# Kernel tuning notes

Hardware: AMD Instinct MI355X
Metric: run time of the kernel (lower is better)

Reference implementation:

```python
import jax, jax.numpy as jnp
import numpy as np

N = 100000      # nodes
E = 1600000     # edges (avg degree 16)
IN, HID, OUT = 128, 32, 64
H = 4           # attention heads in hidden layers

def _p(key, shape, scale=0.1):
    return jax.random.normal(key, shape, dtype=jnp.float32) * scale

def setup_inputs():
    key = jax.random.key(0)
    ks = jax.random.split(key, 16)
    return {
        "x": jax.random.normal(ks[0], (N, IN), dtype=jnp.float32),
        "edge_index": jax.random.randint(ks[1], (2, E), 0, N, dtype=jnp.int32),
        # layer 1: GATConv(IN -> HID, heads=4, concat=True) + BN
        "W1": _p(ks[2], (IN, H * HID)), "as1": _p(ks[3], (H, HID)), "ad1": _p(ks[4], (H, HID)),
        "b1": jnp.zeros((H * HID,), jnp.float32),
        "g1": jnp.ones((H * HID,), jnp.float32), "be1": jnp.zeros((H * HID,), jnp.float32),
        "rm1": _p(ks[5], (H * HID,)), "rv1": jnp.ones((H * HID,), jnp.float32),
        # layer 2: GATConv(H*HID -> HID, heads=4, concat=True) + BN
        "W2": _p(ks[6], (H * HID, H * HID)), "as2": _p(ks[7], (H, HID)), "ad2": _p(ks[8], (H, HID)),
        "b2": jnp.zeros((H * HID,), jnp.float32),
        "g2": jnp.ones((H * HID,), jnp.float32), "be2": jnp.zeros((H * HID,), jnp.float32),
        "rm2": _p(ks[9], (H * HID,)), "rv2": jnp.ones((H * HID,), jnp.float32),
        # layer 3: GATConv(H*HID -> OUT, heads=1, concat=False)
        "W3": _p(ks[10], (H * HID, OUT)), "as3": _p(ks[11], (1, OUT)), "ad3": _p(ks[12], (1, OUT)),
        "b3": jnp.zeros((OUT,), jnp.float32),
    }

def _gat(x, W, a_s, a_d, b, src, dst, heads, ch, concat):
    n = x.shape[0]
    h = (x @ W).reshape(n, heads, ch)                        # [N,H,C]
    e = (h * a_s).sum(-1)[src] + (h * a_d).sum(-1)[dst]      # per-edge logits [E,H]
    e = jax.nn.leaky_relu(e, 0.2)
    m = jax.ops.segment_max(e, dst, num_segments=n)          # segment softmax over dst
    ex = jnp.exp(e - m[dst])
    den = jax.ops.segment_sum(ex, dst, num_segments=n)
    alpha = ex / den[dst]                                    # self loops guarantee den > 0
    out = jax.ops.segment_sum(h[src] * alpha[:, :, None], dst, num_segments=n)
    out = out.reshape(n, heads * ch) if concat else out.mean(axis=1)
    return out + b

def _bn(x, g, b, rm, rv):                                    # BatchNorm1d, eval mode
    return (x - rm) * jax.lax.rsqrt(rv + 1e-5) * g + b

def _forward(x, edge_index, W1, as1, ad1, b1, g1, be1, rm1, rv1,
             W2, as2, ad2, b2, g2, be2, rm2, rv2, W3, as3, ad3, b3):
    n = x.shape[0]
    loop = jnp.arange(n, dtype=edge_index.dtype)             # add self loops (PyG default)
    src = jnp.concatenate([edge_index[0], loop])
    dst = jnp.concatenate([edge_index[1], loop])
    h = _gat(x, W1, as1, ad1, b1, src, dst, H, HID, True)
    h = jax.nn.elu(_bn(h, g1, be1, rm1, rv1))                # dropout = identity (eval)
    h = _gat(h, W2, as2, ad2, b2, src, dst, H, HID, True)
    h = jax.nn.elu(_bn(h, g2, be2, rm2, rv2))
    return _gat(h, W3, as3, ad3, b3, src, dst, 1, OUT, False)

def reference(x, edge_index, W1, as1, ad1, b1, g1, be1, rm1, rv1,
              W2, as2, ad2, b2, g2, be2, rm2, rv2, W3, as3, ad3, b3):
    return _forward(x, edge_index, W1, as1, ad1, b1, g1, be1, rm1, rv1,
                    W2, as2, ad2, b2, g2, be2, rm2, rv2, W3, as3, ad3, b3)
```

## Files before the change

### kernel.cpp

```cpp
#include <hip/hip_runtime.h>
#include <hip/hip_fp16.h>

#define CDIV(a,b) (((a)+(b)-1)/(b))

typedef _Float16 f16x8 __attribute__((ext_vector_type(8)));
typedef float f32x4 __attribute__((ext_vector_type(4)));

__global__ __launch_bounds__(256) void conv_kernel(const float* __restrict__ X,
                                                   __half* __restrict__ Y, int total4) {
  int t = blockIdx.x * blockDim.x + threadIdx.x;
  if (t >= total4) return;
  float4 v = reinterpret_cast<const float4*>(X)[t];
  __half2 a = __floats2half2_rn(v.x, v.y);
  __half2 b = __floats2half2_rn(v.z, v.w);
  reinterpret_cast<__half2*>(Y)[t * 2]     = a;
  reinterpret_cast<__half2*>(Y)[t * 2 + 1] = b;
}

__global__ __launch_bounds__(256) void wprep_kernel(const float* __restrict__ W,
                                                    _Float16* __restrict__ Wt, int NOUT) {
  int i = blockIdx.x * blockDim.x + threadIdx.x;
  if (i >= 128 * NOUT) return;
  int k = i / NOUT, c = i % NOUT;
  int s = k >> 5, g = (k >> 3) & 3, e = k & 7;
  Wt[(size_t)((s * 4 + g) * NOUT + c) * 8 + e] = (_Float16)W[i];
}

template<int NOUT>
__global__ __launch_bounds__(256) void gemm_mfma(const __half* __restrict__ Xh,
                                                 const _Float16* __restrict__ Wt,
                                                 __half* __restrict__ Y, int nrows) {
  constexpr int K = 128;
  constexpr int CT = NOUT / 16;
  const int wave = threadIdx.x >> 6, lane = threadIdx.x & 63;
  const int g = lane >> 4, r16 = lane & 15;
  const int rt = blockIdx.x * 4 + wave;
  if (rt * 16 >= nrows) return;

  const _Float16* xrow = reinterpret_cast<const _Float16*>(Xh)
                         + (size_t)(rt * 16 + r16) * K + g * 8;
  f16x8 a[4];
  #pragma unroll
  for (int s = 0; s < 4; ++s) a[s] = *reinterpret_cast<const f16x8*>(xrow + s * 32);

  f32x4 acc[CT];
  #pragma unroll
  for (int ct = 0; ct < CT; ++ct) acc[ct] = (f32x4){0.f, 0.f, 0.f, 0.f};

  #pragma unroll
  for (int ct = 0; ct < CT; ++ct) {
    #pragma unroll
    for (int s = 0; s < 4; ++s) {
      f16x8 b = *reinterpret_cast<const f16x8*>(&Wt[(size_t)((s * 4 + g) * NOUT + ct * 16 + r16) * 8]);
      acc[ct] = __builtin_amdgcn_mfma_f32_16x16x32_f16(a[s], b, acc[ct], 0, 0, 0);
    }
  }
  const int row0 = rt * 16 + g * 4;
  #pragma unroll
  for (int ct = 0; ct < CT; ++ct) {
    #pragma unroll
    for (int r = 0; r < 4; ++r) {
      Y[(size_t)(row0 + r) * NOUT + ct * 16 + r16] = __float2half_rn(acc[ct][r]);
    }
  }
}

template<int HEADS, int CH>
__global__ __launch_bounds__(256) void scores_kernel(const __half* __restrict__ Hf,
                                                     const float* __restrict__ as_,
                                                     const float* __restrict__ ad_,
                                                     float* __restrict__ ssrc,
                                                     float* __restrict__ sdst, int n) {
  int t = blockIdx.x * blockDim.x + threadIdx.x;
  if (t >= n * HEADS) return;
  int hd = t % HEADS;
  const __half2* hp2 = reinterpret_cast<const __half2*>(Hf + (size_t)t * CH);
  float a = 0.f, b = 0.f;
  #pragma unroll
  for (int c2 = 0; c2 < CH / 2; ++c2) {
    float2 v = __half22float2(hp2[c2]);
    a += v.x * as_[hd * CH + 2 * c2] + v.y * as_[hd * CH + 2 * c2 + 1];
    b += v.x * ad_[hd * CH + 2 * c2] + v.y * ad_[hd * CH + 2 * c2 + 1];
  }
  ssrc[t] = a; sdst[t] = b;
}

__global__ __launch_bounds__(256) void hist_kernel(const int* __restrict__ ei, int E,
                                                   int* __restrict__ deg) {
  int e = blockIdx.x * blockDim.x + threadIdx.x;
  if (e >= E) return;
  atomicAdd(&deg[ei[E + e]], 1);
}

__global__ __launch_bounds__(256) void scan_blocksums(const int* __restrict__ deg,
                                                      int* __restrict__ bsum, int N) {
  __shared__ int red[256];
  int base = blockIdx.x * 1024 + threadIdx.x * 4;
  int s = 0;
  #pragma unroll
  for (int i = 0; i < 4; ++i) { int idx = base + i; if (idx < N) s += deg[idx]; }
  red[threadIdx.x] = s;
  __syncthreads();
  for (int off = 128; off > 0; off >>= 1) {
    if (threadIdx.x < off) red[threadIdx.x] += red[threadIdx.x + off];
    __syncthreads();
  }
  if (threadIdx.x == 0) bsum[blockIdx.x] = red[0];
}

__global__ __launch_bounds__(1024) void scan_bsum(int* __restrict__ bsum, int nb) {
  __shared__ int sh[1024];
  int t = threadIdx.x;
  int v = (t < nb) ? bsum[t] : 0;
  sh[t] = v;
  __syncthreads();
  for (int off = 1; off < 1024; off <<= 1) {
    int tmp = (t >= off) ? sh[t - off] : 0;
    __syncthreads();
    sh[t] += tmp;
    __syncthreads();
  }
  if (t < nb) bsum[t] = sh[t] - v;
}

__global__ __launch_bounds__(256) void scan_final(const int* __restrict__ deg,
                                                  const int* __restrict__ bsum,
                                                  int* __restrict__ rowptr,
                                                  int* __restrict__ cursor, int N) {
  __shared__ int sh[256];
  const int t = threadIdx.x;
  const int base = blockIdx.x * 1024 + t * 4;
  int d[4] = {0, 0, 0, 0};
  #pragma unroll
  for (int i = 0; i < 4; ++i) if (base + i < N) d[i] = deg[base + i];
  int s = d[0] + d[1] + d[2] + d[3];
  sh[t] = s;
  __syncthreads();
  for (int off = 1; off < 256; off <<= 1) {
    int tmp = (t >= off) ? sh[t - off] : 0;
    __syncthreads();
    sh[t] += tmp;
    __syncthreads();
  }
  int run = bsum[blockIdx.x] + sh[t] - s;
  #pragma unroll
  for (int i = 0; i < 4; ++i) {
    if (base + i < N) { rowptr[base + i] = run; cursor[base + i] = run; run += d[i]; }
  }
  if (blockIdx.x == gridDim.x - 1 && t == 255) rowptr[N] = run;
}

__global__ __launch_bounds__(256) void scatter_pass(const int* __restrict__ ei, int E, int N,
                                                    int pw,
                                                    int* __restrict__ cursor,
                                                    int* __restrict__ col) {
  int e = blockIdx.x * blockDim.x + threadIdx.x;
  if (e >= E) return;
  int lo = blockIdx.y * pw;
  int hi = lo + pw;
  int d = ei[E + e];
  if (d < lo || d >= hi) return;
  int pos = atomicAdd(&cursor[d], 1);
  col[pos] = ei[e];
}

template<int HEADS, int CH, bool BN, bool OUTH>
__global__ __launch_bounds__(256) void gat_fused(
    const int* __restrict__ rowptr, const int* __restrict__ col,
    const __half* __restrict__ Hf,
    const float* __restrict__ ssrc, const float* __restrict__ sdst,
    const float* __restrict__ bias, const float* __restrict__ g,
    const float* __restrict__ be, const float* __restrict__ rm,
    const float* __restrict__ rv,
    void* __restrict__ outp, int N) {
  constexpr int NOUT = HEADS * CH;
  constexpr int VEC = NOUT / 64;
  constexpr int SLOTS = 64 / HEADS;
  __shared__ float ptile[4][SLOTS][HEADS];
  __shared__ int   stile[4][SLOTS];
  const int wv = threadIdx.x >> 6, lane = threadIdx.x & 63;
  const int n = blockIdx.x * 4 + wv;
  if (n >= N) return;
  const int eslot = lane / HEADS, head = lane & (HEADS - 1);
  const float sd = sdst[n * HEADS + head];
  float lgs = ssrc[n * HEADS + head] + sd;
  lgs = lgs > 0.f ? lgs : 0.2f * lgs;

  const int c0 = lane * VEC;
  const int hb = c0 / CH;

  float a0, a1 = 0.f;
  if (VEC == 2) {
    float2 hf = __half22float2(*reinterpret_cast<const __half2*>(&Hf[(size_t)n * NOUT + c0]));
    a0 = hf.x; a1 = hf.y;
  } else {
    a0 = __half2float(Hf[(size_t)n * NOUT + c0]);
  }

  float s = 0.f;
  const int beg = rowptr[n], end = rowptr[n + 1];
  for (int base = beg; base < end; base += SLOTS) {
    int e = base + eslot;
    float p = 0.f; int src = 0;
    if (e < end) {
      src = col[e];
      float lg = ssrc[src * HEADS + head] + sd;
      lg = lg > 0.f ? lg : 0.2f * lg;
      p = __expf(lg - lgs);
    }
    ptile[wv][eslot][head] = p;
    if (head == 0) stile[wv][eslot] = src;
    s += p;
    asm volatile("s_waitcnt lgkmcnt(0)" ::: "memory");

    int cnt = min(SLOTS, end - base);
    if (cnt == SLOTS) {
      #pragma unroll 16
      for (int j = 0; j < SLOTS; ++j) {
        int sj = stile[wv][j];
        float pj = ptile[wv][j][hb];
        if (VEC == 2) {
          float2 hf = __half22float2(*reinterpret_cast<const __half2*>(&Hf[(size_t)sj * NOUT + c0]));
          a0 += pj * hf.x; a1 += pj * hf.y;
        } else {
          a0 += pj * __half2float(Hf[(size_t)sj * NOUT + c0]);
        }
      }
    } else {
      for (int j = 0; j < cnt; ++j) {
        int sj = stile[wv][j];
        float pj = ptile[wv][j][hb];
        if (VEC == 2) {
          float2 hf = __half22float2(*reinterpret_cast<const __half2*>(&Hf[(size_t)sj * NOUT + c0]));
          a0 += pj * hf.x; a1 += pj * hf.y;
        } else {
          a0 += pj * __half2float(Hf[(size_t)sj * NOUT + c0]);
        }
      }
    }
  }

  #pragma unroll
  for (int off = HEADS; off < 64; off <<= 1) s += __shfl_xor(s, off);
  float inv = 1.f / (s + 1.f);
  float invb = __shfl(inv, hb);

  float o0 = a0 * invb + bias[c0];
  if (BN) {
    o0 = (o0 - rm[c0]) * rsqrtf(rv[c0] + 1e-5f) * g[c0] + be[c0];
    o0 = o0 > 0.f ? o0 : expm1f(o0);
  }
  if (VEC == 2) {
    float o1 = a1 * invb + bias[c0 + 1];
    if (BN) {
      o1 = (o1 - rm[c0 + 1]) * rsqrtf(rv[c0 + 1] + 1e-5f) * g[c0 + 1] + be[c0 + 1];
      o1 = o1 > 0.f ? o1 : expm1f(o1);
    }
    if (OUTH) {
      __half2 o = __floats2half2_rn(o0, o1);
      *reinterpret_cast<__half2*>(&((__half*)outp)[(size_t)n * NOUT + c0]) = o;
    } else {
      float2 o = make_float2(o0, o1);
      *reinterpret_cast<float2*>(&((float*)outp)[(size_t)n * NOUT + c0]) = o;
    }
  } else {
    if (OUTH) ((__half*)outp)[(size_t)n * NOUT + c0] = __float2half_rn(o0);
    else      ((float*)outp)[(size_t)n * NOUT + c0] = o0;
  }
}

extern "C" void kernel_launch(void* const* d_in, const int* in_sizes, int n_in,
                              void* d_out, int out_size, void* d_ws, size_t ws_size,
                              hipStream_t stream) {
  const float* x   = (const float*)d_in[0];
  const int*   ei  = (const int*)d_in[1];
  const float* W1  = (const float*)d_in[2];
  const float* as1 = (const float*)d_in[3];
  const float* ad1 = (const float*)d_in[4];
  const float* b1  = (const float*)d_in[5];
  const float* g1  = (const float*)d_in[6];
  const float* be1 = (const float*)d_in[7];
  const float* rm1 = (const float*)d_in[8];
  const float* rv1 = (const float*)d_in[9];
  const float* W2  = (const float*)d_in[10];
  const float* as2 = (const float*)d_in[11];
  const float* ad2 = (const float*)d_in[12];
  const float* b2  = (const float*)d_in[13];
  const float* g2  = (const float*)d_in[14];
  const float* be2 = (const float*)d_in[15];
  const float* rm2 = (const float*)d_in[16];
  const float* rv2 = (const float*)d_in[17];
  const float* W3  = (const float*)d_in[18];
  const float* as3 = (const float*)d_in[19];
  const float* ad3 = (const float*)d_in[20];
  const float* b3  = (const float*)d_in[21];

  const int N = in_sizes[0] / 128;
  const int E = in_sizes[1] / 2;
  float* out = (float*)d_out;

  char* p = (char*)d_ws;
  __half* Ah  = (__half*)p;  p += (size_t)N * 128 * 2;
  __half* Bh  = (__half*)p;  p += (size_t)N * 128 * 2;
  float* ssrc = (float*)p;   p += (size_t)N * 4 * 4;
  float* sdst = (float*)p;   p += (size_t)N * 4 * 4;
  int* deg    = (int*)p;     p += (size_t)N * 4;
  int* rowptr = (int*)p;     p += (size_t)(N + 1) * 4;
  int* cursor = (int*)p;     p += (size_t)N * 4;
  int* col    = (int*)p;     p += (size_t)E * 4;
  int* bsum   = (int*)p;     p += 4096;
  _Float16* Wt1 = (_Float16*)p; p += (size_t)128 * 128 * 2;
  _Float16* Wt2 = (_Float16*)p; p += (size_t)128 * 128 * 2;
  _Float16* Wt3 = (_Float16*)p;

  const int fusedB = CDIV(N, 4);
  const int nb = CDIV(N, 1024);
  const int gemmB = CDIV(N, 64);
  constexpr int NPASS = 8;
  const int pw = CDIV(N, NPASS);

  hipMemsetAsync(deg, 0, (size_t)N * sizeof(int), stream);
  hist_kernel<<<CDIV(E, 256), 256, 0, stream>>>(ei, E, deg);
  scan_blocksums<<<nb, 256, 0, stream>>>(deg, bsum, N);
  scan_bsum<<<1, 1024, 0, stream>>>(bsum, nb);
  scan_final<<<nb, 256, 0, stream>>>(deg, bsum, rowptr, cursor, N);
  scatter_pass<<<dim3(CDIV(E, 256), NPASS), 256, 0, stream>>>(ei, E, N, pw, cursor, col);

  wprep_kernel<<<CDIV(128 * 128, 256), 256, 0, stream>>>(W1, Wt1, 128);
  wprep_kernel<<<CDIV(128 * 128, 256), 256, 0, stream>>>(W2, Wt2, 128);
  wprep_kernel<<<CDIV(128 * 64, 256), 256, 0, stream>>>(W3, Wt3, 64);
  conv_kernel<<<CDIV(N * 128 / 4, 256), 256, 0, stream>>>(x, Bh, N * 128 / 4);

  gemm_mfma<128><<<gemmB, 256, 0, stream>>>(Bh, Wt1, Ah, N);
  scores_kernel<4, 32><<<CDIV(N * 4, 256), 256, 0, stream>>>(Ah, as1, ad1, ssrc, sdst, N);
  gat_fused<4, 32, true, true><<<fusedB, 256, 0, stream>>>(rowptr, col, Ah, ssrc, sdst,
                                                           b1, g1, be1, rm1, rv1, Bh, N);

  gemm_mfma<128><<<gemmB, 256, 0, stream>>>(Bh, Wt2, Ah, N);
  scores_kernel<4, 32><<<CDIV(N * 4, 256), 256, 0, stream>>>(Ah, as2, ad2, ssrc, sdst, N);
  gat_fused<4, 32, true, true><<<fusedB, 256, 0, stream>>>(rowptr, col, Ah, ssrc, sdst,
                                                           b2, g2, be2, rm2, rv2, Bh, N);

  gemm_mfma<64><<<gemmB, 256, 0, stream>>>(Bh, Wt3, Ah, N);
  scores_kernel<1, 64><<<CDIV(N, 256), 256, 0, stream>>>(Ah, as3, ad3, ssrc, sdst, N);
  gat_fused<1, 64, false, false><<<fusedB, 256, 0, stream>>>(rowptr, col, Ah, ssrc, sdst,
                                                             b3, b3, b3, b3, b3, out, N);
}
```

Baseline: 489.8 us.

## Fuse score computation into GEMM, fold fp32 conversion, and restructure aggregation with shuffles

The attention-score dot products move into the MFMA GEMM epilogue, computed from the accumulators with cross-lane shuffle reductions. This removes the separate scores kernels and the re-read of the projected features. The layer-1 GEMM now reads fp32 input directly, which drops the standalone conversion kernel, and the three weight-prep launches are merged into one. The aggregation kernel replaces LDS tiles with register shuffles and splits each wave into two halves that process alternate edges with wider per-lane loads, adding the self term at the end; this trades LDS traffic for more shuffles and a final cross-half reduction.

```diff
diff --git a/kernel.cpp b/kernel.cpp
--- a/kernel.cpp
+++ b/kernel.cpp
@@ -1,47 +1,63 @@
 #include <hip/hip_runtime.h>
 #include <hip/hip_fp16.h>
+#include <type_traits>
 
 #define CDIV(a,b) (((a)+(b)-1)/(b))
 
 typedef _Float16 f16x8 __attribute__((ext_vector_type(8)));
 typedef float f32x4 __attribute__((ext_vector_type(4)));
 
-__global__ __launch_bounds__(256) void conv_kernel(const float* __restrict__ X,
-                                                   __half* __restrict__ Y, int total4) {
-  int t = blockIdx.x * blockDim.x + threadIdx.x;
-  if (t >= total4) return;
-  float4 v = reinterpret_cast<const float4*>(X)[t];
-  __half2 a = __floats2half2_rn(v.x, v.y);
-  __half2 b = __floats2half2_rn(v.z, v.w);
-  reinterpret_cast<__half2*>(Y)[t * 2]     = a;
-  reinterpret_cast<__half2*>(Y)[t * 2 + 1] = b;
-}
-
-__global__ __launch_bounds__(256) void wprep_kernel(const float* __restrict__ W,
-                                                    _Float16* __restrict__ Wt, int NOUT) {
-  int i = blockIdx.x * blockDim.x + threadIdx.x;
-  if (i >= 128 * NOUT) return;
+__device__ __forceinline__ void wxform(const float* __restrict__ W,
+                                       _Float16* __restrict__ Wt, int i, int NOUT) {
   int k = i / NOUT, c = i % NOUT;
   int s = k >> 5, g = (k >> 3) & 3, e = k & 7;
   Wt[(size_t)((s * 4 + g) * NOUT + c) * 8 + e] = (_Float16)W[i];
 }
-
-template<int NOUT>
-__global__ __launch_bounds__(256) void gemm_mfma(const __half* __restrict__ Xh,
-                                                 const _Float16* __restrict__ Wt,
-                                                 __half* __restrict__ Y, int nrows) {
+__global__ __launch_bounds__(256) void wprep_all(const float* __restrict__ W1,
+                                                 const float* __restrict__ W2,
+                                                 const float* __restrict__ W3,
+                                                 _Float16* __restrict__ Wt1,
+                                                 _Float16* __restrict__ Wt2,
+                                                 _Float16* __restrict__ Wt3) {
+  int i = blockIdx.x * blockDim.x + threadIdx.x;
+  if (i < 128 * 128) { wxform(W1, Wt1, i, 128); wxform(W2, Wt2, i, 128); }
+  if (i < 128 * 64)  { wxform(W3, Wt3, i, 64); }
+}
+
+template<typename AT>
+__device__ __forceinline__ f16x8 load_afrag(const AT* __restrict__ xrow) {
+  if constexpr (std::is_same<AT, _Float16>::value) {
+    return *reinterpret_cast<const f16x8*>(xrow);
+  } else {
+    float4 v0 = *reinterpret_cast<const float4*>(xrow);
+    float4 v1 = *reinterpret_cast<const float4*>(xrow + 4);
+    f16x8 r = {(_Float16)v0.x, (_Float16)v0.y, (_Float16)v0.z, (_Float16)v0.w,
+               (_Float16)v1.x, (_Float16)v1.y, (_Float16)v1.z, (_Float16)v1.w};
+    return r;
+  }
+}
+
+template<int NOUT, int HEADS, typename AT>
+__global__ __launch_bounds__(256) void gemm_sc(const AT* __restrict__ X,
+                                               const _Float16* __restrict__ Wt,
+                                               const float* __restrict__ as_,
+                                               const float* __restrict__ ad_,
+                                               __half* __restrict__ Y,
+                                               float* __restrict__ ssrc,
+                                               float* __restrict__ sdst, int nrows) {
   constexpr int K = 128;
   constexpr int CT = NOUT / 16;
+  constexpr int CH = NOUT / HEADS;
+  constexpr int CPH = CH / 16;
   const int wave = threadIdx.x >> 6, lane = threadIdx.x & 63;
   const int g = lane >> 4, r16 = lane & 15;
   const int rt = blockIdx.x * 4 + wave;
   if (rt * 16 >= nrows) return;
 
-  const _Float16* xrow = reinterpret_cast<const _Float16*>(Xh)
-                         + (size_t)(rt * 16 + r16) * K + g * 8;
+  const AT* xrow = X + (size_t)(rt * 16 + r16) * K + g * 8;
   f16x8 a[4];
   #pragma unroll
-  for (int s = 0; s < 4; ++s) a[s] = *reinterpret_cast<const f16x8*>(xrow + s * 32);
+  for (int s = 0; s < 4; ++s) a[s] = load_afrag(xrow + s * 32);
 
   f32x4 acc[CT];
   #pragma unroll
@@ -63,26 +79,47 @@
       Y[(size_t)(row0 + r) * NOUT + ct * 16 + r16] = __float2half_rn(acc[ct][r]);
     }
   }
-}
-
-template<int HEADS, int CH>
-__global__ __launch_bounds__(256) void scores_kernel(const __half* __restrict__ Hf,
-                                                     const float* __restrict__ as_,
-                                                     const float* __restrict__ ad_,
-                                                     float* __restrict__ ssrc,
-                                                     float* __restrict__ sdst, int n) {
-  int t = blockIdx.x * blockDim.x + threadIdx.x;
-  if (t >= n * HEADS) return;
-  int hd = t % HEADS;
-  const __half2* hp2 = reinterpret_cast<const __half2*>(Hf + (size_t)t * CH);
-  float a = 0.f, b = 0.f;
-  #pragma unroll
-  for (int c2 = 0; c2 < CH / 2; ++c2) {
-    float2 v = __half22float2(hp2[c2]);
-    a += v.x * as_[hd * CH + 2 * c2] + v.y * as_[hd * CH + 2 * c2 + 1];
-    b += v.x * ad_[hd * CH + 2 * c2] + v.y * ad_[hd * CH + 2 * c2 + 1];
-  }
-  ssrc[t] = a; sdst[t] = b;
+
+  float pas[4][HEADS], pad_[4][HEADS];
+  #pragma unroll
+  for (int r = 0; r < 4; ++r)
+    #pragma unroll
+    for (int h = 0; h < HEADS; ++h) { pas[r][h] = 0.f; pad_[r][h] = 0.f; }
+  #pragma unroll
+  for (int h = 0; h < HEADS; ++h) {
+    #pragma unroll
+    for (int q = 0; q < CPH; ++q) {
+      float asv = as_[h * CH + q * 16 + r16];
+      float adv = ad_[h * CH + q * 16 + r16];
+      #pragma unroll
+      for (int r = 0; r < 4; ++r) {
+        float av = acc[h * CPH + q][r];
+        pas[r][h] += av * asv;
+        pad_[r][h] += av * adv;
+      }
+    }
+  }
+  #pragma unroll
+  for (int off = 1; off < 16; off <<= 1) {
+    #pragma unroll
+    for (int r = 0; r < 4; ++r)
+      #pragma unroll
+      for (int h = 0; h < HEADS; ++h) {
+        pas[r][h] += __shfl_xor(pas[r][h], off);
+        pad_[r][h] += __shfl_xor(pad_[r][h], off);
+      }
+  }
+  #pragma unroll
+  for (int h = 0; h < HEADS; ++h) {
+    if (r16 == h) {
+      #pragma unroll
+      for (int r = 0; r < 4; ++r) ssrc[(size_t)(row0 + r) * HEADS + h] = pas[r][h];
+    }
+    if (r16 == 8 + h) {
+      #pragma unroll
+      for (int r = 0; r < 4; ++r) sdst[(size_t)(row0 + r) * HEADS + h] = pad_[r][h];
+    }
+  }
 }
 
 __global__ __launch_bounds__(256) void hist_kernel(const int* __restrict__ ei, int E,
@@ -165,7 +202,7 @@
 }
 
 template<int HEADS, int CH, bool BN, bool OUTH>
-__global__ __launch_bounds__(256) void gat_fused(
+__global__ __launch_bounds__(256) void gat_fused2(
     const int* __restrict__ rowptr, const int* __restrict__ col,
     const __half* __restrict__ Hf,
     const float* __restrict__ ssrc, const float* __restrict__ sdst,
@@ -174,98 +211,100 @@
     const float* __restrict__ rv,
     void* __restrict__ outp, int N) {
   constexpr int NOUT = HEADS * CH;
-  constexpr int VEC = NOUT / 64;
   constexpr int SLOTS = 64 / HEADS;
-  __shared__ float ptile[4][SLOTS][HEADS];
-  __shared__ int   stile[4][SLOTS];
+  constexpr int CPL = NOUT / 32;
   const int wv = threadIdx.x >> 6, lane = threadIdx.x & 63;
   const int n = blockIdx.x * 4 + wv;
   if (n >= N) return;
   const int eslot = lane / HEADS, head = lane & (HEADS - 1);
+  const int half_ = lane >> 5, li = lane & 31;
+  const int c0 = li * CPL;
+  const int hb = c0 / CH;
+
   const float sd = sdst[n * HEADS + head];
   float lgs = ssrc[n * HEADS + head] + sd;
   lgs = lgs > 0.f ? lgs : 0.2f * lgs;
 
-  const int c0 = lane * VEC;
-  const int hb = c0 / CH;
-
-  float a0, a1 = 0.f;
-  if (VEC == 2) {
-    float2 hf = __half22float2(*reinterpret_cast<const __half2*>(&Hf[(size_t)n * NOUT + c0]));
-    a0 = hf.x; a1 = hf.y;
-  } else {
-    a0 = __half2float(Hf[(size_t)n * NOUT + c0]);
-  }
-
-  float s = 0.f;
+  float a[CPL];
+  #pragma unroll
+  for (int c = 0; c < CPL; ++c) a[c] = 0.f;
+
+  float ssum = 0.f;
   const int beg = rowptr[n], end = rowptr[n + 1];
   for (int base = beg; base < end; base += SLOTS) {
     int e = base + eslot;
-    float p = 0.f; int src = 0;
+    float p = 0.f; int srcv = 0;
     if (e < end) {
-      src = col[e];
-      float lg = ssrc[src * HEADS + head] + sd;
+      srcv = col[e];
+      float lg = ssrc[srcv * HEADS + head] + sd;
       lg = lg > 0.f ? lg : 0.2f * lg;
       p = __expf(lg - lgs);
     }
-    ptile[wv][eslot][head] = p;
-    if (head == 0) stile[wv][eslot] = src;
-    s += p;
-    asm volatile("s_waitcnt lgkmcnt(0)" ::: "memory");
+    ssum += p;
 
     int cnt = min(SLOTS, end - base);
-    if (cnt == SLOTS) {
-      #pragma unroll 16
-      for (int j = 0; j < SLOTS; ++j) {
-        int sj = stile[wv][j];
-        float pj = ptile[wv][j][hb];
-        if (VEC == 2) {
-          float2 hf = __half22float2(*reinterpret_cast<const __half2*>(&Hf[(size_t)sj * NOUT + c0]));
-          a0 += pj * hf.x; a1 += pj * hf.y;
-        } else {
-          a0 += pj * __half2float(Hf[(size_t)sj * NOUT + c0]);
-        }
+    int nstep = (cnt + 1) >> 1;
+    #pragma unroll 4
+    for (int step = 0; step < nstep; ++step) {
+      int j = step * 2 + half_;
+      int sl = j * HEADS + hb;
+      float pj = __shfl(p, sl);
+      int sj = __shfl(srcv, sl);
+      const __half* hp = Hf + (size_t)sj * NOUT + c0;
+      if constexpr (CPL == 4) {
+        float2 raw = *reinterpret_cast<const float2*>(hp);
+        float2 f01 = __half22float2(*reinterpret_cast<const __half2*>(&raw.x));
+        float2 f23 = __half22float2(*reinterpret_cast<const __half2*>(&raw.y));
+        a[0] += pj * f01.x; a[1] += pj * f01.y;
+        a[2] += pj * f23.x; a[3] += pj * f23.y;
+      } else {
+        float2 f01 = __half22float2(*reinterpret_cast<const __half2*>(hp));
+        a[0] += pj * f01.x; a[1] += pj * f01.y;
+      }
+    }
+  }
+
+  #pragma unroll
+  for (int off = HEADS; off < 64; off <<= 1) ssum += __shfl_xor(ssum, off);
+  float inv = 1.f / (ssum + 1.f);
+  float invb = __shfl(inv, hb);
+
+  #pragma unroll
+  for (int c = 0; c < CPL; ++c) a[c] += __shfl_xor(a[c], 32);
+
+  if (half_ == 0) {
+    const __half* hp = Hf + (size_t)n * NOUT + c0;
+    float o[CPL];
+    #pragma unroll
+    for (int c = 0; c < CPL; ++c) {
+      a[c] += __half2float(hp[c]);
+      o[c] = a[c] * invb + bias[c0 + c];
+      if (BN) {
+        o[c] = (o[c] - rm[c0 + c]) * rsqrtf(rv[c0 + c] + 1e-5f) * g[c0 + c] + be[c0 + c];
+        o[c] = o[c] > 0.f ? o[c] : expm1f(o[c]);
+      }
+    }
+    if (OUTH) {
+      __half* op = (__half*)outp + (size_t)n * NOUT + c0;
+      if constexpr (CPL == 4) {
+        __half2 o01 = __floats2half2_rn(o[0], o[1]);
+        __half2 o23 = __floats2half2_rn(o[2], o[3]);
+        float2 st;
+        st.x = *reinterpret_cast<float*>(&o01);
+        st.y = *reinterpret_cast<float*>(&o23);
+        *reinterpret_cast<float2*>(op) = st;
+      } else {
+        __half2 o01 = __floats2half2_rn(o[0], o[1]);
+        *reinterpret_cast<__half2*>(op) = o01;
       }
     } else {
-      for (int j = 0; j < cnt; ++j) {
-        int sj = stile[wv][j];
-        float pj = ptile[wv][j][hb];
-        if (VEC == 2) {
-          float2 hf = __half22float2(*reinterpret_cast<const __half2*>(&Hf[(size_t)sj * NOUT + c0]));
-          a0 += pj * hf.x; a1 += pj * hf.y;
-        } else {
-          a0 += pj * __half2float(Hf[(size_t)sj * NOUT + c0]);
-        }
-      }
-    }
-  }
-
-  #pragma unroll
-  for (int off = HEADS; off < 64; off <<= 1) s += __shfl_xor(s, off);
-  float inv = 1.f / (s + 1.f);
-  float invb = __shfl(inv, hb);
-
-  float o0 = a0 * invb + bias[c0];
-  if (BN) {
-    o0 = (o0 - rm[c0]) * rsqrtf(rv[c0] + 1e-5f) * g[c0] + be[c0];
-    o0 = o0 > 0.f ? o0 : expm1f(o0);
-  }
-  if (VEC == 2) {
-    float o1 = a1 * invb + bias[c0 + 1];
-    if (BN) {
-      o1 = (o1 - rm[c0 + 1]) * rsqrtf(rv[c0 + 1] + 1e-5f) * g[c0 + 1] + be[c0 + 1];
-      o1 = o1 > 0.f ? o1 : expm1f(o1);
-    }
-    if (OUTH) {
-      __half2 o = __floats2half2_rn(o0, o1);
-      *reinterpret_cast<__half2*>(&((__half*)outp)[(size_t)n * NOUT + c0]) = o;
-    } else {
-      float2 o = make_float2(o0, o1);
-      *reinterpret_cast<float2*>(&((float*)outp)[(size_t)n * NOUT + c0]) = o;
-    }
-  } else {
-    if (OUTH) ((__half*)outp)[(size_t)n * NOUT + c0] = __float2half_rn(o0);
-    else      ((float*)outp)[(size_t)n * NOUT + c0] = o0;
+      float* op = (float*)outp + (size_t)n * NOUT + c0;
+      if constexpr (CPL == 4) {
+        *reinterpret_cast<float4*>(op) = make_float4(o[0], o[1], o[2], o[3]);
+      } else {
+        *reinterpret_cast<float2*>(op) = make_float2(o[0], o[1]);
+      }
+    }
   }
 }
 
@@ -326,23 +365,19 @@
   scan_final<<<nb, 256, 0, stream>>>(deg, bsum, rowptr, cursor, N);
   scatter_pass<<<dim3(CDIV(E, 256), NPASS), 256, 0, stream>>>(ei, E, N, pw, cursor, col);
 
-  wprep_kernel<<<CDIV(128 * 128, 256), 256, 0, stream>>>(W1, Wt1, 128);
-  wprep_kernel<<<CDIV(128 * 128, 256), 256, 0, stream>>>(W2, Wt2, 128);
-  wprep_kernel<<<CDIV(128 * 64, 256), 256, 0, stream>>>(W3, Wt3, 64);
-  conv_kernel<<<CDIV(N * 128 / 4, 256), 256, 0, stream>>>(x, Bh, N * 128 / 4);
-
-  gemm_mfma<128><<<gemmB, 256, 0, stream>>>(Bh, Wt1, Ah, N);
-  scores_kernel<4, 32><<<CDIV(N * 4, 256), 256, 0, stream>>>(Ah, as1, ad1, ssrc, sdst, N);
-  gat_fused<4, 32, true, true><<<fusedB, 256, 0, stream>>>(rowptr, col, Ah, ssrc, sdst,
-                                                           b1, g1, be1, rm1, rv1, Bh, N);
-
-  gemm_mfma<128><<<gemmB, 256, 0, stream>>>(Bh, Wt2, Ah, N);
-  scores_kernel<4, 32><<<CDIV(N * 4, 256), 256, 0, stream>>>(Ah, as2, ad2, ssrc, sdst, N);
-  gat_fused<4, 32, true, true><<<fusedB, 256, 0, stream>>>(rowptr, col, Ah, ssrc, sdst,
-                                                           b2, g2, be2, rm2, rv2, Bh, N);
-
-  gemm_mfma<64><<<gemmB, 256, 0, stream>>>(Bh, Wt3, Ah, N);
-  scores_kernel<1, 64><<<CDIV(N, 256), 256, 0, stream>>>(Ah, as3, ad3, ssrc, sdst, N);
-  gat_fused<1, 64, false, false><<<fusedB, 256, 0, stream>>>(rowptr, col, Ah, ssrc, sdst,
-                                                             b3, b3, b3, b3, b3, out, N);
-}
+  wprep_all<<<CDIV(128 * 128, 256), 256, 0, stream>>>(W1, W2, W3, Wt1, Wt2, Wt3);
+
+  gemm_sc<128, 4, float><<<gemmB, 256, 0, stream>>>(x, Wt1, as1, ad1, Ah, ssrc, sdst, N);
+  gat_fused2<4, 32, true, true><<<fusedB, 256, 0, stream>>>(rowptr, col, Ah, ssrc, sdst,
+                                                            b1, g1, be1, rm1, rv1, Bh, N);
+
+  gemm_sc<128, 4, _Float16><<<gemmB, 256, 0, stream>>>((const _Float16*)Bh, Wt2, as2, ad2,
+                                                       Ah, ssrc, sdst, N);
+  gat_fused2<4, 32, true, true><<<fusedB, 256, 0, stream>>>(rowptr, col, Ah, ssrc, sdst,
+                                                            b2, g2, be2, rm2, rv2, Bh, N);
+
+  gemm_sc<64, 1, _Float16><<<gemmB, 256, 0, stream>>>((const _Float16*)Bh, Wt3, as3, ad3,
+                                                      Ah, ssrc, sdst, N);
+  gat_fused2<1, 64, false, false><<<fusedB, 256, 0, stream>>>(rowptr, col, Ah, ssrc, sdst,
+                                                              b3, b3, b3, b3, b3, out, N);
+}
```

After: 533.3 us. 1.09x slower.
